# Kernel optimization log

Hardware: AMD Instinct MI355X
Metric: run time of the kernel (lower is better)

Reference implementation:

```python
import math
import jax, jax.numpy as jnp
import numpy as np

NEG = -1e32
H = 8          # n_heads
L2 = 1e-05


def _ln(x, g, b):
    m = jnp.mean(x, -1, keepdims=True)
    v = jnp.mean((x - m) ** 2, -1, keepdims=True)
    return g * (x - m) * jax.lax.rsqrt(v + 1e-5) + b


def _attn(q, k, v, gam, mask_k, zero_pad):
    # q,k,v: [B,H,S,d]; monotonic distance-decay attention (AKT style)
    d_k = q.shape[-1]
    S = q.shape[2]
    scores = jnp.einsum('bhqd,bhkd->bhqk', q, k) / math.sqrt(d_k)
    # torch: triu(ones, k=mask)==0  ->  tril(0) if mask_k==1 else tril(-1)
    mask = jnp.tril(jnp.ones((S, S), bool), 0 if mask_k == 1 else -1)[None, None]
    # first (detached) softmax, used only to build the distance effect
    s_ = jax.nn.softmax(jnp.where(mask, scores, NEG), -1) * mask
    distcum = jnp.cumsum(s_, -1)
    disttot = jnp.sum(s_, -1, keepdims=True)
    idx = jnp.arange(S, dtype=jnp.float32)
    pos = jnp.abs(idx[None, :] - idx[:, None])[None, None]  # |j - i|
    dist = jax.lax.stop_gradient(
        jnp.sqrt(jnp.clip((disttot - distcum) * pos, 0.0, None)))
    gamma = -jax.nn.softplus(gam)[None]  # [1,H,1,1], gam is learned
    total_effect = jnp.clip(jnp.exp(dist * gamma), 1e-5, 1e5)
    scores = jax.nn.softmax(jnp.where(mask, scores * total_effect, NEG), -1)
    if zero_pad:
        scores = scores.at[:, :, 0, :].set(0.0)
    return jnp.einsum('bhqk,bhkd->bhqd', scores, v)


def _mha(qi, ki, vi, kW, kb, vW, vb, oW, ob, gam, mask_k, zero_pad):
    # kq_same=True: q and k both use k_linear
    B, S = qi.shape[:2]
    sp = lambda x: x.reshape(B, S, H, -1).transpose(0, 2, 1, 3)
    q = sp(qi @ kW + kb)
    k = sp(ki @ kW + kb)
    v = sp(vi @ vW + vb)
    o = _attn(q, k, v, gam, mask_k, zero_pad)
    o = o.transpose(0, 2, 1, 3).reshape(B, S, -1)
    return o @ oW + ob


def _tlayer(query, key, values, mask_k, zero_pad, apply_pos,
            kW, kb, vW, vb, oW, ob, gam, ln1g, ln1b,
            f1W, f1b, f2W, f2b, ln2g, ln2b):
    q2 = _mha(query, key, values, kW, kb, vW, vb, oW, ob, gam, mask_k, zero_pad)
    x = _ln(query + q2, ln1g, ln1b)
    if apply_pos:
        ff = jax.nn.relu(x @ f1W + f1b) @ f2W + f2b
        x = _ln(x + ff, ln2g, ln2b)
    return x


def _forward(p_data, pa_data, target, pemb_W, diff_W, qemb_W, qemb_b,
             y_kW, y_kb, y_vW, y_vb, y_oW, y_ob, y_gam, y_ln1g, y_ln1b,
             y_f1W, y_f1b, y_f2W, y_f2b, y_ln2g, y_ln2b,
             x_kW, x_kb, x_vW, x_vb, x_oW, x_ob, x_gam, x_ln1g, x_ln1b,
             h_kW, h_kb, h_vW, h_vb, h_oW, h_ob, h_gam, h_ln1g, h_ln1b,
             h_f1W, h_f1b, h_f2W, h_f2b, h_ln2g, h_ln2b,
             oln1g, oln1b, o1W, o1b, oln2g, oln2b, o2W, o2b,
             oln3g, oln3b, o3W, o3b):
    NPID = pemb_W.shape[0] - 1

    def qe(qd):  # q_embed: Linear -> ReLU, normalized by row-sum of q_data
        return jax.nn.relu(qd @ qemb_W + qemb_b) / jnp.sum(qd, -1, keepdims=True)

    q_data = jax.nn.sigmoid(pemb_W[p_data])           # [B,S,NQ+1]
    q_embed = qe(q_data)                              # [B,S,D]
    pa_pos = jnp.where(pa_data > NPID, pa_data - NPID, 0)
    pa_neg = jnp.where(pa_data <= NPID, pa_data, 0)
    qa_pos = jax.nn.sigmoid(pemb_W[pa_pos])
    qa_neg = jax.nn.sigmoid(pemb_W[pa_neg])
    qa_embed = jnp.concatenate([qe(qa_pos), qe(qa_neg)], -1)  # [B,S,2D]
    pid = diff_W[p_data]                              # [B,S,1]
    q_embed = q_embed + pid
    qa_embed = qa_embed + pid
    c_reg = jnp.sum(pid ** 2) * L2

    # Architecture (n_blocks = 1)
    y = _tlayer(qa_embed, qa_embed, qa_embed, 1, False, True,
                y_kW, y_kb, y_vW, y_vb, y_oW, y_ob, y_gam, y_ln1g, y_ln1b,
                y_f1W, y_f1b, y_f2W, y_f2b, y_ln2g, y_ln2b)
    x = _tlayer(q_embed, q_embed, q_embed, 1, False, False,
                x_kW, x_kb, x_vW, x_vb, x_oW, x_ob, x_gam, x_ln1g, x_ln1b,
                None, None, None, None, None, None)
    x = _tlayer(x, x, y, 0, True, True,
                h_kW, h_kb, h_vW, h_vb, h_oW, h_ob, h_gam, h_ln1g, h_ln1b,
                h_f1W, h_f1b, h_f2W, h_f2b, h_ln2g, h_ln2b)

    c = jnp.concatenate([x, q_embed], -1)             # [B,S,2D]
    o = jax.nn.relu(_ln(c, oln1g, oln1b) @ o1W + o1b)
    o = jax.nn.relu(_ln(o, oln2g, oln2b) @ o2W + o2b)
    out = _ln(o, oln3g, oln3b) @ o3W + o3b            # [B,S,1]
    return out, c_reg


def setup_inputs():
    B, S, D, NQ, NPID, FC, DFF = 8, 1024, 256, 1024, 4096, 512, 2048
    key = jax.random.key(0)
    cnt = [0]

    def nk():
        cnt[0] += 1
        return jax.random.fold_in(key, cnt[0])

    def nrm(shape, s=0.05):
        return jax.random.normal(nk(), shape, dtype=jnp.float32) * s

    z = lambda sh: jnp.zeros(sh, jnp.float32)
    on = lambda sh: jnp.ones(sh, jnp.float32)

    return dict(
        p_data=jax.random.randint(nk(), (B, S), 0, NPID + 1),
        pa_data=jax.random.randint(nk(), (B, S), 0, 2 * NPID + 1),
        target=jax.random.uniform(nk(), (B, S), jnp.float32),
        pemb_W=nrm((NPID + 1, NQ + 1), 1.0), diff_W=nrm((NPID + 1, 1), 0.1),
        qemb_W=nrm((NQ + 1, D)), qemb_b=z((D,)),
        y_kW=nrm((2 * D, 2 * D)), y_kb=z((2 * D,)),
        y_vW=nrm((2 * D, 2 * D)), y_vb=z((2 * D,)),
        y_oW=nrm((2 * D, 2 * D)), y_ob=z((2 * D,)), y_gam=nrm((H, 1, 1), 1.0),
        y_ln1g=on((2 * D,)), y_ln1b=z((2 * D,)),
        y_f1W=nrm((2 * D, DFF)), y_f1b=z((DFF,)),
        y_f2W=nrm((DFF, 2 * D)), y_f2b=z((2 * D,)),
        y_ln2g=on((2 * D,)), y_ln2b=z((2 * D,)),
        x_kW=nrm((D, D)), x_kb=z((D,)), x_vW=nrm((D, D)), x_vb=z((D,)),
        x_oW=nrm((D, D)), x_ob=z((D,)), x_gam=nrm((H, 1, 1), 1.0),
        x_ln1g=on((D,)), x_ln1b=z((D,)),
        h_kW=nrm((D, D)), h_kb=z((D,)),
        h_vW=nrm((2 * D, 2 * D)), h_vb=z((2 * D,)),
        h_oW=nrm((2 * D, D)), h_ob=z((D,)), h_gam=nrm((H, 1, 1), 1.0),
        h_ln1g=on((D,)), h_ln1b=z((D,)),
        h_f1W=nrm((D, DFF)), h_f1b=z((DFF,)),
        h_f2W=nrm((DFF, D)), h_f2b=z((D,)),
        h_ln2g=on((D,)), h_ln2b=z((D,)),
        oln1g=on((2 * D,)), oln1b=z((2 * D,)),
        o1W=nrm((2 * D, FC)), o1b=z((FC,)),
        oln2g=on((FC,)), oln2b=z((FC,)),
        o2W=nrm((FC, 256)), o2b=z((256,)),
        oln3g=on((256,)), oln3b=z((256,)),
        o3W=nrm((256, 1)), o3b=z((1,)),
    )


def reference(p_data, pa_data, target, pemb_W, diff_W, qemb_W, qemb_b,
              y_kW, y_kb, y_vW, y_vb, y_oW, y_ob, y_gam, y_ln1g, y_ln1b,
              y_f1W, y_f1b, y_f2W, y_f2b, y_ln2g, y_ln2b,
              x_kW, x_kb, x_vW, x_vb, x_oW, x_ob, x_gam, x_ln1g, x_ln1b,
              h_kW, h_kb, h_vW, h_vb, h_oW, h_ob, h_gam, h_ln1g, h_ln1b,
              h_f1W, h_f1b, h_f2W, h_f2b, h_ln2g, h_ln2b,
              oln1g, oln1b, o1W, o1b, oln2g, oln2b, o2W, o2b,
              oln3g, oln3b, o3W, o3b):
    return _forward(p_data, pa_data, target, pemb_W, diff_W, qemb_W, qemb_b,
                    y_kW, y_kb, y_vW, y_vb, y_oW, y_ob, y_gam, y_ln1g, y_ln1b,
                    y_f1W, y_f1b, y_f2W, y_f2b, y_ln2g, y_ln2b,
                    x_kW, x_kb, x_vW, x_vb, x_oW, x_ob, x_gam, x_ln1g, x_ln1b,
                    h_kW, h_kb, h_vW, h_vb, h_oW, h_ob, h_gam, h_ln1g, h_ln1b,
                    h_f1W, h_f1b, h_f2W, h_f2b, h_ln2g, h_ln2b,
                    oln1g, oln1b, o1W, o1b, oln2g, oln2b, o2W, o2b,
                    oln3g, oln3b, o3W, o3b)
```

## Files before the change

### kernel.cpp

```cpp
#include <hip/hip_runtime.h>
#include <hip/hip_bf16.h>
#include <math.h>

#define NHEADS 8
#define L2E 1.44269504f

typedef __attribute__((ext_vector_type(8))) __bf16 bfrag;
typedef __attribute__((ext_vector_type(4))) float f32x4;
typedef __attribute__((ext_vector_type(8))) unsigned short u16x8;

static __device__ __forceinline__ unsigned short f2bf(float f) {
  unsigned u = __float_as_uint(f);
  unsigned r = (u + 0x7fffu + ((u >> 16) & 1u)) >> 16;
  return (unsigned short)r;
}

static __device__ __forceinline__ void gload_lds16(const void* g, void* l) {
  __builtin_amdgcn_global_load_lds(
      (const __attribute__((address_space(1))) unsigned int*)g,
      (__attribute__((address_space(3))) unsigned int*)l, 16, 0, 0);
}

static __device__ __forceinline__ float block_reduce_sum(float v, float* red) {
  int t = threadIdx.x;
  red[t] = v; __syncthreads();
  for (int s = 128; s > 0; s >>= 1) {
    if (t < s) red[t] += red[t + s];
    __syncthreads();
  }
  float r = red[0];
  __syncthreads();
  return r;
}

__global__ __launch_bounds__(256) void sig_kernel(
    const float* __restrict__ Wp, unsigned short* __restrict__ Sgb,
    float* __restrict__ Ssum, int Kd, int Kp)
{
  __shared__ float red[256];
  int row = blockIdx.x;
  float s = 0.f;
  for (int k = threadIdx.x; k < Kp; k += 256) {
    float v = 0.f;
    if (k < Kd) {
      v = 1.f / (1.f + __expf(-Wp[(size_t)row * Kd + k]));
      s += v;
    }
    Sgb[(size_t)row * Kp + k] = f2bf(v);
  }
  float tot = block_reduce_sum(s, red);
  if (threadIdx.x == 0) Ssum[row] = tot;
}

struct TDesc { const float* src; unsigned short* dst; int K, N, Kp, tilesX, blk0; };
struct TPack { TDesc d[16]; };

__global__ __launch_bounds__(256) void tconv_all_kernel(TPack P) {
  __shared__ float t[32][33];
  int bid = blockIdx.x;
  int di = 0;
  #pragma unroll
  for (int k = 1; k < 16; ++k) if (bid >= P.d[k].blk0) di = k;
  const float* src = P.d[di].src;
  unsigned short* dst = P.d[di].dst;
  int K = P.d[di].K, N = P.d[di].N, Kp = P.d[di].Kp, tilesX = P.d[di].tilesX;
  int local = bid - P.d[di].blk0;
  int bn = (local % tilesX) * 32;
  int bk = (local / tilesX) * 32;
  int tid = threadIdx.x;
  int tx = tid & 31, ty = tid >> 5;
  #pragma unroll
  for (int u = 0; u < 4; ++u) {
    int k = bk + ty + u * 8, n = bn + tx;
    t[ty + u * 8][tx] = (k < K && n < N) ? src[(size_t)k * N + n] : 0.f;
  }
  __syncthreads();
  #pragma unroll
  for (int u = 0; u < 4; ++u) {
    int n = bn + ty + u * 8, kk = bk + tx;
    if (n < N && kk < Kp)
      dst[(size_t)n * Kp + kk] = f2bf(t[tx][ty + u * 8]);
  }
}

template<int BM, int EPI, bool WF32, bool WBF, bool WTR>
__global__ __launch_bounds__(256) void mgemm_kernel(
    const unsigned short* __restrict__ A, const unsigned short* __restrict__ Bt,
    const float* __restrict__ bias, float* __restrict__ C,
    unsigned short* __restrict__ Cb, unsigned short* __restrict__ Ct,
    int M, int N, int K, const float* __restrict__ divv,
    const float* __restrict__ bias2, int Nk)
{
  constexpr int TN  = (BM == 128) ? 128 : 64;
  constexpr int NI  = (BM == 128) ? 4 : 2;
  constexpr int NJ  = (BM == 128) ? 4 : 2;
  constexpr int WSM = (BM == 128) ? 64 : 32;
  constexpr bool SPLIT = WBF && WTR;
  __shared__ __align__(16) unsigned short Als[BM * 32];
  __shared__ __align__(16) unsigned short Bls[TN * 32];
  const int tid = threadIdx.x;
  const int lane = tid & 63, w = tid >> 6;
  const int wm = w >> 1, wn = w & 1;
  const int brow = blockIdx.y * BM, bcol = blockIdx.x * TN;

  f32x4 acc[NI][NJ] = {};

  for (int k0 = 0; k0 < K; k0 += 32) {
    if constexpr (BM == 128) {
      #pragma unroll
      for (int q = 0; q < 2; ++q) {
        int s = w * 128 + q * 64 + lane;
        int r = s >> 2, g = s & 3;
        int gs = g ^ (r & 3);
        int gc = bcol + r; if (gc > N - 1) gc = N - 1;
        gload_lds16(Bt + (size_t)gc * K + k0 + gs * 8,
                    (char*)Bls + (w * 2048 + q * 1024));
      }
      #pragma unroll
      for (int q = 0; q < 2; ++q) {
        int s = w * 128 + q * 64 + lane;
        int r = s >> 2, g = s & 3;
        int gs = g ^ (r & 3);
        int gr = brow + r; if (gr > M - 1) gr = M - 1;
        gload_lds16(A + (size_t)gr * K + k0 + gs * 8,
                    (char*)Als + (w * 2048 + q * 1024));
      }
    } else {
      {
        int s = tid;
        int r = s >> 2, g = s & 3;
        int gs = g ^ (r & 3);
        int gc = bcol + r; if (gc > N - 1) gc = N - 1;
        gload_lds16(Bt + (size_t)gc * K + k0 + gs * 8,
                    (char*)Bls + w * 1024);
      }
      {
        int s = tid;
        int r = s >> 2, g = s & 3;
        int gs = g ^ (r & 3);
        int gr = brow + r; if (gr > M - 1) gr = M - 1;
        gload_lds16(A + (size_t)gr * K + k0 + gs * 8,
                    (char*)Als + w * 1024);
      }
    }
    __syncthreads();

    bfrag av[NI], bv[NJ];
    #pragma unroll
    for (int f = 0; f < NI; ++f) {
      int rA = wm * WSM + f * 16 + (lane & 15);
      av[f] = *(const bfrag*)((const char*)Als + rA * 64 + ((((lane >> 4) ^ (rA & 3))) << 4));
    }
    #pragma unroll
    for (int f = 0; f < NJ; ++f) {
      int rB = wn * WSM + f * 16 + (lane & 15);
      bv[f] = *(const bfrag*)((const char*)Bls + rB * 64 + ((((lane >> 4) ^ (rB & 3))) << 4));
    }
    #pragma unroll
    for (int i = 0; i < NI; ++i)
      #pragma unroll
      for (int j = 0; j < NJ; ++j)
        acc[i][j] = __builtin_amdgcn_mfma_f32_16x16x32_bf16(av[i], bv[j], acc[i][j], 0, 0, 0);
    __syncthreads();
  }

  #pragma unroll
  for (int i = 0; i < NI; ++i) {
    int gr0 = brow + wm * WSM + i * 16 + (lane >> 4) * 4;
    #pragma unroll
    for (int j = 0; j < NJ; ++j) {
      int gc = bcol + wn * WSM + j * 16 + (lane & 15);
      float bsv;
      if (SPLIT) bsv = (gc < Nk) ? bias[gc] : bias2[gc - Nk];
      else       bsv = bias ? bias[gc] : 0.f;
      float vv[4];
      #pragma unroll
      for (int q = 0; q < 4; ++q) {
        int gr = gr0 + q;
        float v = acc[i][j][q] + bsv;
        if (EPI >= 1) v = fmaxf(v, 0.f);
        if (EPI == 2) v = (gr < M) ? v / divv[gr] : v;
        vv[q] = v;
      }
      if (SPLIT) {
        if (gc < Nk) {
          #pragma unroll
          for (int q = 0; q < 4; ++q) {
            int gr = gr0 + q;
            if (gr < M) Cb[(size_t)gr * Nk + gc] = f2bf(vv[q]);
          }
        } else {
          ushort4 h4 = { f2bf(vv[0]), f2bf(vv[1]), f2bf(vv[2]), f2bf(vv[3]) };
          *(ushort4*)(Ct + (size_t)(gc - Nk) * M + gr0) = h4;
        }
      } else {
        #pragma unroll
        for (int q = 0; q < 4; ++q) {
          int gr = gr0 + q;
          if (gr >= M) continue;
          if (WF32) C[(size_t)gr * N + gc] = vv[q];
          if (WBF)  Cb[(size_t)gr * N + gc] = f2bf(vv[q]);
        }
        if (WTR) {
          ushort4 h4 = { f2bf(vv[0]), f2bf(vv[1]), f2bf(vv[2]), f2bf(vv[3]) };
          *(ushort4*)(Ct + (size_t)gc * M + gr0) = h4;
        }
      }
    }
  }
}

__global__ __launch_bounds__(256) void gather_kernel(
    const int* __restrict__ p_data, const int* __restrict__ pa_data,
    const float* __restrict__ E, const float* __restrict__ diff_W,
    float* __restrict__ qemb, unsigned short* __restrict__ qembb,
    float* __restrict__ qaemb, unsigned short* __restrict__ qaembb)
{
  int idx = blockIdx.x * 256 + threadIdx.x;
  if (idx >= 8192 * 512) return;
  int row = idx >> 9, c = idx & 511;
  int p = p_data[row];
  float pid = diff_W[p];
  if (c < 256) {
    float v = E[(size_t)p * 256 + c] + pid;
    qemb[(size_t)row * 256 + c] = v;
    qembb[(size_t)row * 256 + c] = f2bf(v);
  }
  int pa = pa_data[row];
  int ppos = (pa > 4096) ? pa - 4096 : 0;
  int pneg = (pa <= 4096) ? pa : 0;
  float v = (c < 256) ? E[(size_t)ppos * 256 + c] : E[(size_t)pneg * 256 + (c - 256)];
  v += pid;
  qaemb[(size_t)row * 512 + c] = v;
  qaembb[(size_t)row * 512 + c] = f2bf(v);
}

__global__ __launch_bounds__(256) void creg_kernel(
    const int* __restrict__ p_data, const float* __restrict__ dW,
    float* __restrict__ out)
{
  __shared__ float red[256];
  float s = 0.f;
  for (int i = threadIdx.x; i < 8192; i += 256) {
    float v = dW[p_data[i]];
    s += v * v;
  }
  float tot = block_reduce_sum(s, red);
  if (threadIdx.x == 0) out[0] = tot * 1e-5f;
}

template<int DK, int DV, int MASKK, int ZP>
__global__ __launch_bounds__(512, 4) void attnA_kernel(
    const unsigned short* __restrict__ QKb, const unsigned short* __restrict__ Vt,
    const float* __restrict__ gamp, unsigned short* __restrict__ O,
    int S, int MT)
{
  constexpr int RS = 1156;
  constexpr int HIOFF = 2048;
  constexpr int NPAR = (DV == 64) ? 2 : 4;
  constexpr int NFIN = (DV == 64) ? 4 : 2;
  constexpr int NP   = (DV == 32) ? 6 : 4;
  const int DMK = NHEADS * DK, DMV = NHEADS * DV;
  const int id = blockIdx.x + blockIdx.y * 64;
  const int W = (id & 7) * 512 + (id >> 3);
  const int ib = 63 - (W & 63);
  const int bh = W >> 6;
  const int i0 = ib * 16;
  const int b = bh >> 3, h = bh & 7;
  const int tid = threadIdx.x;
  const int lane = tid & 63, w = tid >> 6;
  const size_t rowbase = (size_t)b * S;

  __shared__ __align__(16) float sc[16 * RS];
  __shared__ float wrow[16];

  const int jmaxBlk = MASKK ? (i0 + 15) : (i0 + 14);
  const int NK = (jmaxBlk / 64 + 1) * 64;
  const int NKp = (NK + 255) & ~255;
  const int CD = NKp >> 5;

  const int qr = lane & 15;
  const int ko8 = (lane >> 4) * 8;
  const float rscale = rsqrtf((float)DK) * L2E;

  bfrag qf[DK / 32];
  #pragma unroll
  for (int ks = 0; ks < DK / 32; ++ks)
    qf[ks] = *(const bfrag*)(QKb + (rowbase + i0 + qr) * DMK + h * DK + ks * 32 + ko8);

  for (int t0 = 0; t0 < NK; t0 += 128) {
    int tt = t0 + (w >> 2) * 64;
    if (tt < NK) {
      int jb = tt + (w & 3) * 16 + qr;
      bfrag kf[DK / 32];
      #pragma unroll
      for (int ks = 0; ks < DK / 32; ++ks)
        kf[ks] = *(const bfrag*)(QKb + (rowbase + jb) * DMK + h * DK + ks * 32 + ko8);
      f32x4 accs = {};
      __builtin_amdgcn_s_setprio(1);
      #pragma unroll
      for (int ks = 0; ks < DK / 32; ++ks)
        accs = __builtin_amdgcn_mfma_f32_16x16x32_bf16(qf[ks], kf[ks], accs, 0, 0, 0);
      __builtin_amdgcn_s_setprio(0);
      int ja = jb + 4 * (jb >> 5);
      int r0 = (lane >> 4) * 4;
      #pragma unroll
      for (int q = 0; q < 4; ++q)
        sc[(r0 + q) * RS + ja] = accs[q] * rscale;
    }
  }
  __syncthreads();

  {
    const int g = tid >> 5, l = tid & 31;
    const int i = i0 + g;
    const int jmax = MASKK ? i : i - 1;
    const int jb0 = CD * l;

    float p[32];
    float m1 = -1e30f;
    #pragma unroll
    for (int c = 0; c < 8; ++c) {
      if (4 * c < CD) {
        int j = jb0 + 4 * c;
        f32x4 v = *(const f32x4*)(sc + g * RS + j + 4 * (j >> 5));
        #pragma unroll
        for (int k = 0; k < 4; ++k) {
          int jj = j + k;
          float s = (jj <= jmax) ? v[k] : -1e30f;
          p[4 * c + k] = s;
          m1 = fmaxf(m1, s);
        }
      }
    }
    #pragma unroll
    for (int o = 16; o > 0; o >>= 1) m1 = fmaxf(m1, __shfl_xor(m1, o, 32));

    float lloc = 0.f;
    #pragma unroll
    for (int t = 0; t < 32; ++t)
      if (t < CD) lloc += __builtin_amdgcn_exp2f(p[t] - m1);
    float l1 = lloc;
    #pragma unroll
    for (int o = 16; o > 0; o >>= 1) l1 += __shfl_xor(l1, o, 32);

    float scn = lloc;
    #pragma unroll
    for (int o = 1; o < 32; o <<= 1) {
      float u = __shfl_up(scn, o, 32);
      if (l >= o) scn += u;
    }
    float cum = scn - lloc;

    float gv = gamp[h];
    float sp = fmaxf(gv, 0.f) + log1pf(__expf(-fabsf(gv)));
    float gmr = -sp * L2E * rsqrtf(l1);
    float dj = (float)(i - jb0);
    float m2 = -1e30f;
    #pragma unroll
    for (int t = 0; t < 32; ++t) {
      if (t < CD) {
        cum += __builtin_amdgcn_exp2f(p[t] - m1);
        float rem = fmaxf(l1 - cum, 0.f);
        float dsq = sqrtf(rem * fabsf(dj));
        dj -= 1.f;
        float eff = fmaxf(__builtin_amdgcn_exp2f(gmr * dsq), 1e-5f);
        p[t] = p[t] * eff;
        m2 = fmaxf(m2, p[t]);
      }
    }
    #pragma unroll
    for (int o = 16; o > 0; o >>= 1) m2 = fmaxf(m2, __shfl_xor(m2, o, 32));

    float l2 = 0.f;
    #pragma unroll
    for (int t = 0; t < 32; ++t)
      if (t < CD) { p[t] = __builtin_amdgcn_exp2f(p[t] - m2); l2 += p[t]; }
    #pragma unroll
    for (int o = 16; o > 0; o >>= 1) l2 += __shfl_xor(l2, o, 32);
    bool validrow = (jmax >= 0) && !(ZP && i == 0);
    float wgt = validrow ? (1.f / l2) : 0.f;
    if (l == 0) wrow[g] = wgt;

    char* rowB = (char*)sc + (size_t)g * (RS * 4);
    #pragma unroll
    for (int k = 0; k < 4; ++k) {
      if (8 * k < CD) {
        int bb = (CD >> 3) * l + k;
        int pb = ((bb & 3) << 5) | (bb >> 2);
        u16x8 hi8, lo8;
        #pragma unroll
        for (int e = 0; e < 8; ++e) {
          float v = p[8 * k + e];
          __bf16 hb = (__bf16)v;
          hi8[e] = __builtin_bit_cast(unsigned short, hb);
          lo8[e] = __builtin_bit_cast(unsigned short, (__bf16)(v - (float)hb));
        }
        *(u16x8*)(rowB + 16 * pb) = hi8;
        *(u16x8*)(rowB + HIOFF + 16 * pb) = lo8;
      }
    }
  }
  __syncthreads();

  const int dblk = (DV == 64) ? (w & 3) : (w & 1);
  const int par  = (DV == 64) ? (w >> 2) : (w >> 1);
  const int dcol = h * DV + dblk * 16 + (lane & 15);
  const unsigned short* vrow = Vt + (size_t)dcol * MT + rowbase;
  f32x4 acco = {};
  const char* rowB = (const char*)sc + (size_t)qr * (RS * 4);
  __builtin_amdgcn_s_setprio(1);
  for (int t0 = par * 64; t0 < NK; t0 += NPAR * 64) {
    #pragma unroll
    for (int ks = 0; ks < 2; ++ks) {
      int jo = t0 + ks * 32 + ko8;
      int bb = jo >> 3;
      int pb = ((bb & 3) << 5) | (bb >> 2);
      bfrag ph = *(const bfrag*)(rowB + 16 * pb);
      bfrag pl = *(const bfrag*)(rowB + HIOFF + 16 * pb);
      bfrag vf = *(const bfrag*)(vrow + jo);
      acco = __builtin_amdgcn_mfma_f32_16x16x32_bf16(pl, vf, acco, 0, 0, 0);
      acco = __builtin_amdgcn_mfma_f32_16x16x32_bf16(ph, vf, acco, 0, 0, 0);
    }
  }
  __builtin_amdgcn_s_setprio(0);
  __syncthreads();

  float* redA = sc;
  if (w >= NFIN) {
    int slot = w - NFIN;
    #pragma unroll
    for (int q = 0; q < 4; ++q)
      redA[slot * 272 + ((lane >> 4) * 4 + q) * 17 + (lane & 15)] = acco[q];
  }
  __syncthreads();
  if (w < NFIN) {
    for (int pp = w; pp < NP; pp += NFIN) {
      #pragma unroll
      for (int q = 0; q < 4; ++q)
        acco[q] += redA[pp * 272 + ((lane >> 4) * 4 + q) * 17 + (lane & 15)];
    }
    int r0 = (lane >> 4) * 4;
    #pragma unroll
    for (int q = 0; q < 4; ++q) {
      float wv = wrow[r0 + q];
      O[(rowbase + i0 + r0 + q) * DMV + dcol] = f2bf(acco[q] * wv);
    }
  }
}

template<int D, bool WF, bool WB>
__global__ __launch_bounds__(256) void ln4_kernel(
    const float* __restrict__ X, const float* __restrict__ R,
    const float* __restrict__ g, const float* __restrict__ be,
    float* __restrict__ Y, unsigned short* __restrict__ Yb)
{
  constexpr int NC = D / 256;
  int row = blockIdx.x * 4 + (threadIdx.x >> 6);
  int lane = threadIdx.x & 63;
  const float* x = X + (size_t)row * D;
  f32x4 xv[NC];
  float s = 0.f;
  #pragma unroll
  for (int c = 0; c < NC; ++c) {
    xv[c] = *(const f32x4*)(x + c * 256 + lane * 4);
    if (R) {
      f32x4 rv = *(const f32x4*)(R + (size_t)row * D + c * 256 + lane * 4);
      #pragma unroll
      for (int k = 0; k < 4; ++k) xv[c][k] += rv[k];
    }
    #pragma unroll
    for (int k = 0; k < 4; ++k) s += xv[c][k];
  }
  #pragma unroll
  for (int o = 32; o > 0; o >>= 1) s += __shfl_xor(s, o, 64);
  float mean = s / (float)D;
  float vs = 0.f;
  #pragma unroll
  for (int c = 0; c < NC; ++c)
    #pragma unroll
    for (int k = 0; k < 4; ++k) { float d = xv[c][k] - mean; vs += d * d; }
  #pragma unroll
  for (int o = 32; o > 0; o >>= 1) vs += __shfl_xor(vs, o, 64);
  float rstd = rsqrtf(vs / (float)D + 1e-5f);
  #pragma unroll
  for (int c = 0; c < NC; ++c) {
    f32x4 gv = *(const f32x4*)(g + c * 256 + lane * 4);
    f32x4 bv = *(const f32x4*)(be + c * 256 + lane * 4);
    f32x4 ov;
    #pragma unroll
    for (int k = 0; k < 4; ++k) ov[k] = gv[k] * (xv[c][k] - mean) * rstd + bv[k];
    if (WF) *(f32x4*)(Y + (size_t)row * D + c * 256 + lane * 4) = ov;
    if (WB) {
      ushort4 h4 = { f2bf(ov[0]), f2bf(ov[1]), f2bf(ov[2]), f2bf(ov[3]) };
      *(ushort4*)(Yb + (size_t)row * D + c * 256 + lane * 4) = h4;
    }
  }
}

__global__ __launch_bounds__(256) void lnc_kernel(
    const float* __restrict__ Xh, const float* __restrict__ Qe,
    const float* __restrict__ g, const float* __restrict__ be,
    unsigned short* __restrict__ Yb)
{
  int row = blockIdx.x * 4 + (threadIdx.x >> 6);
  int lane = threadIdx.x & 63;
  f32x4 xv[2];
  xv[0] = *(const f32x4*)(Xh + (size_t)row * 256 + lane * 4);
  xv[1] = *(const f32x4*)(Qe + (size_t)row * 256 + lane * 4);
  float s = 0.f;
  #pragma unroll
  for (int c = 0; c < 2; ++c)
    #pragma unroll
    for (int k = 0; k < 4; ++k) s += xv[c][k];
  #pragma unroll
  for (int o = 32; o > 0; o >>= 1) s += __shfl_xor(s, o, 64);
  float mean = s / 512.f;
  float vs = 0.f;
  #pragma unroll
  for (int c = 0; c < 2; ++c)
    #pragma unroll
    for (int k = 0; k < 4; ++k) { float d = xv[c][k] - mean; vs += d * d; }
  #pragma unroll
  for (int o = 32; o > 0; o >>= 1) vs += __shfl_xor(vs, o, 64);
  float rstd = rsqrtf(vs / 512.f + 1e-5f);
  #pragma unroll
  for (int c = 0; c < 2; ++c) {
    f32x4 gv = *(const f32x4*)(g + c * 256 + lane * 4);
    f32x4 bv = *(const f32x4*)(be + c * 256 + lane * 4);
    ushort4 h4;
    #pragma unroll
    for (int k = 0; k < 4; ++k) {
      float ov = gv[k] * (xv[c][k] - mean) * rstd + bv[k];
      ((unsigned short*)&h4)[k] = f2bf(ov);
    }
    *(ushort4*)(Yb + (size_t)row * 512 + c * 256 + lane * 4) = h4;
  }
}

__global__ __launch_bounds__(256) void lndot_kernel(
    const float* __restrict__ X, const float* __restrict__ g,
    const float* __restrict__ be, const float* __restrict__ w3,
    const float* __restrict__ b3, float* __restrict__ out)
{
  int row = blockIdx.x * 4 + (threadIdx.x >> 6);
  int lane = threadIdx.x & 63;
  f32x4 v = *(const f32x4*)(X + (size_t)row * 256 + lane * 4);
  float s = v[0] + v[1] + v[2] + v[3];
  #pragma unroll
  for (int o = 32; o > 0; o >>= 1) s += __shfl_xor(s, o, 64);
  float mean = s / 256.f;
  float vs = 0.f;
  #pragma unroll
  for (int k = 0; k < 4; ++k) { float d = v[k] - mean; vs += d * d; }
  #pragma unroll
  for (int o = 32; o > 0; o >>= 1) vs += __shfl_xor(vs, o, 64);
  float rstd = rsqrtf(vs / 256.f + 1e-5f);
  f32x4 gv = *(const f32x4*)(g + lane * 4);
  f32x4 bv = *(const f32x4*)(be + lane * 4);
  f32x4 wv = *(const f32x4*)(w3 + lane * 4);
  float d = 0.f;
  #pragma unroll
  for (int k = 0; k < 4; ++k)
    d += (gv[k] * (v[k] - mean) * rstd + bv[k]) * wv[k];
  #pragma unroll
  for (int o = 32; o > 0; o >>= 1) d += __shfl_xor(d, o, 64);
  if (lane == 0) out[row] = d + b3[0];
}

extern "C" void kernel_launch(void* const* d_in, const int* in_sizes, int n_in,
                              void* d_out, int out_size, void* d_ws, size_t ws_size,
                              hipStream_t stream) {
  const int* p_data  = (const int*)d_in[0];
  const int* pa_data = (const int*)d_in[1];
  const float* pemb_W = (const float*)d_in[3];
  const float* diff_W = (const float*)d_in[4];
  const float* qemb_W = (const float*)d_in[5];
  const float* qemb_b = (const float*)d_in[6];
  const float* y_kW = (const float*)d_in[7];   const float* y_kb = (const float*)d_in[8];
  const float* y_vW = (const float*)d_in[9];   const float* y_vb = (const float*)d_in[10];
  const float* y_oW = (const float*)d_in[11];  const float* y_ob = (const float*)d_in[12];
  const float* y_gam = (const float*)d_in[13];
  const float* y_ln1g = (const float*)d_in[14]; const float* y_ln1b = (const float*)d_in[15];
  const float* y_f1W = (const float*)d_in[16]; const float* y_f1b = (const float*)d_in[17];
  const float* y_f2W = (const float*)d_in[18]; const float* y_f2b = (const float*)d_in[19];
  const float* y_ln2g = (const float*)d_in[20]; const float* y_ln2b = (const float*)d_in[21];
  const float* x_kW = (const float*)d_in[22];  const float* x_kb = (const float*)d_in[23];
  const float* x_vW = (const float*)d_in[24];  const float* x_vb = (const float*)d_in[25];
  const float* x_oW = (const float*)d_in[26];  const float* x_ob = (const float*)d_in[27];
  const float* x_gam = (const float*)d_in[28];
  const float* x_ln1g = (const float*)d_in[29]; const float* x_ln1b = (const float*)d_in[30];
  const float* h_kW = (const float*)d_in[31];  const float* h_kb = (const float*)d_in[32];
  const float* h_vW = (const float*)d_in[33];  const float* h_vb = (const float*)d_in[34];
  const float* h_oW = (const float*)d_in[35];  const float* h_ob = (const float*)d_in[36];
  const float* h_gam = (const float*)d_in[37];
  const float* h_ln1g = (const float*)d_in[38]; const float* h_ln1b = (const float*)d_in[39];
  const float* h_f1W = (const float*)d_in[40]; const float* h_f1b = (const float*)d_in[41];
  const float* h_f2W = (const float*)d_in[42]; const float* h_f2b = (const float*)d_in[43];
  const float* h_ln2g = (const float*)d_in[44]; const float* h_ln2b = (const float*)d_in[45];
  const float* oln1g = (const float*)d_in[46]; const float* oln1b = (const float*)d_in[47];
  const float* o1W = (const float*)d_in[48];   const float* o1b = (const float*)d_in[49];
  const float* oln2g = (const float*)d_in[50]; const float* oln2b = (const float*)d_in[51];
  const float* o2W = (const float*)d_in[52];   const float* o2b = (const float*)d_in[53];
  const float* oln3g = (const float*)d_in[54]; const float* oln3b = (const float*)d_in[55];
  const float* o3W = (const float*)d_in[56];   const float* o3b = (const float*)d_in[57];

  float* out_f = (float*)d_out;

  const int B = 8, S = 1024, M = B * S;
  const int R = 4097, KQ = 1025, KQP = 1056;

  float* ws = (float*)d_ws;
  size_t off = 0;
  auto alloc = [&](size_t nfloats) { size_t o = off; off += (nfloats + 255) & ~(size_t)255; return o; };
  auto allocs = [&](size_t nshorts) { return alloc((nshorts + 1) / 2); };

  size_t oE    = alloc((size_t)R * 256);
  size_t oSIGb = allocs((size_t)R * KQP);
  size_t oSSUM = alloc(R);
  size_t oQE   = alloc((size_t)M * 256);
  size_t oQEb  = allocs((size_t)M * 256);
  size_t oQA   = alloc((size_t)M * 512);
  size_t oQAb  = allocs((size_t)M * 512);
  size_t oYOb  = allocs((size_t)M * 512);
  size_t oXO   = alloc((size_t)M * 256);
  size_t oXOb  = allocs((size_t)M * 256);
  size_t oHO   = alloc((size_t)M * 256);
  size_t oS0   = alloc((size_t)M * 512);
  size_t oS1   = alloc((size_t)M * 512);
  size_t oS2b  = allocs((size_t)M * 512);
  size_t oS3   = alloc((size_t)M * 512);
  size_t oS4   = alloc((size_t)M * 512);
  size_t oSX   = alloc((size_t)M * 512);
  size_t oSXb  = allocs((size_t)M * 512);
  size_t oS0b  = allocs((size_t)M * 512);
  size_t oVt   = allocs((size_t)M * 512);
  size_t oWqe  = allocs((size_t)256 * KQP);
  size_t oWyk  = allocs((size_t)512 * 512);
  size_t oWyv  = allocs((size_t)512 * 512);
  size_t oWyo  = allocs((size_t)512 * 512);
  size_t oWyf1 = allocs((size_t)2048 * 512);
  size_t oWyf2 = allocs((size_t)512 * 2048);
  size_t oWxk  = allocs((size_t)256 * 256);
  size_t oWxv  = allocs((size_t)256 * 256);
  size_t oWxo  = allocs((size_t)256 * 256);
  size_t oWhk  = allocs((size_t)256 * 256);
  size_t oWhv  = allocs((size_t)512 * 512);
  size_t oWho  = allocs((size_t)256 * 512);
  size_t oWhf1 = allocs((size_t)2048 * 256);
  size_t oWhf2 = allocs((size_t)256 * 2048);
  size_t oWo1  = allocs((size_t)512 * 512);
  size_t oWo2  = allocs((size_t)256 * 512);
  (void)ws_size; (void)in_sizes; (void)n_in; (void)out_size;

  float* E    = ws + oE;
  unsigned short* SIGb = (unsigned short*)(ws + oSIGb);
  float* SSUM = ws + oSSUM;
  float* QE   = ws + oQE;   unsigned short* QEb = (unsigned short*)(ws + oQEb);
  float* QA   = ws + oQA;   unsigned short* QAb = (unsigned short*)(ws + oQAb);
  unsigned short* YOb = (unsigned short*)(ws + oYOb);
  float* XO   = ws + oXO;   unsigned short* XOb = (unsigned short*)(ws + oXOb);
  float* HO   = ws + oHO;
  float* S0   = ws + oS0;
  unsigned short* S2b = (unsigned short*)(ws + oS2b);
  float* S3   = ws + oS3;
  float* S4   = ws + oS4;
  float* SX   = ws + oSX;   unsigned short* SXb = (unsigned short*)(ws + oSXb);
  unsigned short* S0b = (unsigned short*)(ws + oS0b);
  unsigned short* Vt  = (unsigned short*)(ws + oVt);
  unsigned short* FFb = (unsigned short*)S0;

  unsigned short* Wqe  = (unsigned short*)(ws + oWqe);
  unsigned short* Wyk  = (unsigned short*)(ws + oWyk);
  unsigned short* Wyv  = (unsigned short*)(ws + oWyv);
  unsigned short* Wyo  = (unsigned short*)(ws + oWyo);
  unsigned short* Wyf1 = (unsigned short*)(ws + oWyf1);
  unsigned short* Wyf2 = (unsigned short*)(ws + oWyf2);
  unsigned short* Wxk  = (unsigned short*)(ws + oWxk);
  unsigned short* Wxv  = (unsigned short*)(ws + oWxv);
  unsigned short* Wxo  = (unsigned short*)(ws + oWxo);
  unsigned short* Whk  = (unsigned short*)(ws + oWhk);
  unsigned short* Whv  = (unsigned short*)(ws + oWhv);
  unsigned short* Who  = (unsigned short*)(ws + oWho);
  unsigned short* Whf1 = (unsigned short*)(ws + oWhf1);
  unsigned short* Whf2 = (unsigned short*)(ws + oWhf2);
  unsigned short* Wo1  = (unsigned short*)(ws + oWo1);
  unsigned short* Wo2  = (unsigned short*)(ws + oWo2);

  dim3 blk(256);
  int nElem512 = (8192 * 512 + 255) / 256;

  {
    struct HD { const float* src; unsigned short* dst; int K, N, Kp; };
    const HD hd[16] = {
      {qemb_W, Wqe, KQ, 256, KQP},
      {y_kW, Wyk, 512, 512, 512}, {y_vW, Wyv, 512, 512, 512}, {y_oW, Wyo, 512, 512, 512},
      {y_f1W, Wyf1, 512, 2048, 512}, {y_f2W, Wyf2, 2048, 512, 2048},
      {x_kW, Wxk, 256, 256, 256}, {x_vW, Wxv, 256, 256, 256}, {x_oW, Wxo, 256, 256, 256},
      {h_kW, Whk, 256, 256, 256}, {h_vW, Whv, 512, 512, 512}, {h_oW, Who, 512, 256, 512},
      {h_f1W, Whf1, 256, 2048, 256}, {h_f2W, Whf2, 2048, 256, 2048},
      {o1W, Wo1, 512, 512, 512}, {o2W, Wo2, 512, 256, 512},
    };
    TPack P;
    int tot = 0;
    for (int k = 0; k < 16; ++k) {
      int tx = (hd[k].N + 31) / 32, ty = (hd[k].Kp + 31) / 32;
      P.d[k] = { hd[k].src, hd[k].dst, hd[k].K, hd[k].N, hd[k].Kp, tx, tot };
      tot += tx * ty;
    }
    tconv_all_kernel<<<dim3(tot), blk, 0, stream>>>(P);
  }

  auto gg128 = [](int Mm, int Nn) { return dim3((unsigned)(Nn / 128), (unsigned)((Mm + 127) / 128)); };
  auto gg64  = [](int Mm, int Nn) { return dim3((unsigned)(Nn / 64), (unsigned)((Mm + 63) / 64)); };

  sig_kernel<<<R, blk, 0, stream>>>(pemb_W, SIGb, SSUM, KQ, KQP);
  mgemm_kernel<64, 2, true, false, false><<<gg64(R, 256), blk, 0, stream>>>(SIGb, Wqe, qemb_b, E, nullptr, nullptr, R, 256, KQP, SSUM, nullptr, 0);
  gather_kernel<<<nElem512, blk, 0, stream>>>(p_data, pa_data, E, diff_W, QE, QEb, QA, QAb);
  creg_kernel<<<1, blk, 0, stream>>>(p_data, diff_W, out_f + 8192);

  dim3 ablk(512);
  dim3 lgrid(M / 4);
  dim3 agA(64, B * NHEADS);

  mgemm_kernel<64, 0, false, true, true><<<gg64(M, 1024), blk, 0, stream>>>(QAb, Wyk, y_kb, nullptr, S0b, Vt, M, 1024, 512, nullptr, y_vb, 512);
  attnA_kernel<64, 64, 1, 0><<<agA, ablk, 0, stream>>>(S0b, Vt, y_gam, S2b, S, M);
  mgemm_kernel<64, 0, true, false, false><<<gg64(M, 512), blk, 0, stream>>>(S2b, Wyo, y_ob, S3, nullptr, nullptr, M, 512, 512, nullptr, nullptr, 0);
  ln4_kernel<512, true, true><<<lgrid, blk, 0, stream>>>(QA, S3, y_ln1g, y_ln1b, SX, SXb);
  mgemm_kernel<128, 1, false, true, false><<<gg128(M, 2048), blk, 0, stream>>>(SXb, Wyf1, y_f1b, nullptr, FFb, nullptr, M, 2048, 512, nullptr, nullptr, 0);
  mgemm_kernel<128, 0, true, false, false><<<gg128(M, 512), blk, 0, stream>>>(FFb, Wyf2, y_f2b, S4, nullptr, nullptr, M, 512, 2048, nullptr, nullptr, 0);
  ln4_kernel<512, false, true><<<lgrid, blk, 0, stream>>>(SX, S4, y_ln2g, y_ln2b, nullptr, YOb);

  mgemm_kernel<64, 0, false, true, true><<<gg64(M, 512), blk, 0, stream>>>(QEb, Wxk, x_kb, nullptr, S0b, Vt, M, 512, 256, nullptr, x_vb, 256);
  attnA_kernel<32, 32, 1, 0><<<agA, ablk, 0, stream>>>(S0b, Vt, x_gam, S2b, S, M);
  mgemm_kernel<64, 0, true, false, false><<<gg64(M, 256), blk, 0, stream>>>(S2b, Wxo, x_ob, S3, nullptr, nullptr, M, 256, 256, nullptr, nullptr, 0);
  ln4_kernel<256, true, true><<<lgrid, blk, 0, stream>>>(QE, S3, x_ln1g, x_ln1b, XO, XOb);

  mgemm_kernel<64, 0, false, true, false><<<gg64(M, 256), blk, 0, stream>>>(XOb, Whk, h_kb, nullptr, S0b, nullptr, M, 256, 256, nullptr, nullptr, 0);
  mgemm_kernel<64, 0, false, false, true><<<gg64(M, 512), blk, 0, stream>>>(YOb, Whv, h_vb, nullptr, nullptr, Vt, M, 512, 512, nullptr, nullptr, 0);
  attnA_kernel<32, 64, 0, 1><<<agA, ablk, 0, stream>>>(S0b, Vt, h_gam, S2b, S, M);
  mgemm_kernel<64, 0, true, false, false><<<gg64(M, 256), blk, 0, stream>>>(S2b, Who, h_ob, S3, nullptr, nullptr, M, 256, 512, nullptr, nullptr, 0);
  ln4_kernel<256, true, true><<<lgrid, blk, 0, stream>>>(XO, S3, h_ln1g, h_ln1b, SX, SXb);
  mgemm_kernel<128, 1, false, true, false><<<gg128(M, 2048), blk, 0, stream>>>(SXb, Whf1, h_f1b, nullptr, FFb, nullptr, M, 2048, 256, nullptr, nullptr, 0);
  mgemm_kernel<64, 0, true, false, false><<<gg64(M, 256), blk, 0, stream>>>(FFb, Whf2, h_f2b, S4, nullptr, nullptr, M, 256, 2048, nullptr, nullptr, 0);
  ln4_kernel<256, true, false><<<lgrid, blk, 0, stream>>>(SX, S4, h_ln2g, h_ln2b, HO, nullptr);

  lnc_kernel<<<lgrid, blk, 0, stream>>>(HO, QE, oln1g, oln1b, SXb);
  mgemm_kernel<64, 1, true, false, false><<<gg64(M, 512), blk, 0, stream>>>(SXb, Wo1, o1b, S3, nullptr, nullptr, M, 512, 512, nullptr, nullptr, 0);
  ln4_kernel<512, false, true><<<lgrid, blk, 0, stream>>>(S3, nullptr, oln2g, oln2b, nullptr, SXb);
  mgemm_kernel<64, 1, true, false, false><<<gg64(M, 256), blk, 0, stream>>>(SXb, Wo2, o2b, S4, nullptr, nullptr, M, 256, 512, nullptr, nullptr, 0);
  lndot_kernel<<<lgrid, blk, 0, stream>>>(S4, oln3g, oln3b, o3W, o3b, out_f);
}
```

Baseline: 747.8 us.

## Stream attention softmax through LDS and add 128x64 GEMM tile shape

The attention kernel no longer holds the per-row score array in registers. It rereads scores from shared memory in each softmax pass, writes the decayed scores back in place, and then stores the bf16 hi/lo probabilities interleaved in the same row buffer. The aim is to cut register pressure and the separate packed-layout region, at the cost of more LDS traffic. The GEMM template also gains an independent TN parameter, so several projections now use 128x64 tiles instead of 64x64, which changes per-block reuse and grid size.

```diff
diff --git a/kernel.cpp b/kernel.cpp
--- a/kernel.cpp
+++ b/kernel.cpp
@@ -83,7 +83,7 @@
   }
 }
 
-template<int BM, int EPI, bool WF32, bool WBF, bool WTR>
+template<int BM, int TN, int EPI, bool WF32, bool WBF, bool WTR>
 __global__ __launch_bounds__(256) void mgemm_kernel(
     const unsigned short* __restrict__ A, const unsigned short* __restrict__ Bt,
     const float* __restrict__ bias, float* __restrict__ C,
@@ -91,10 +91,8 @@
     int M, int N, int K, const float* __restrict__ divv,
     const float* __restrict__ bias2, int Nk)
 {
-  constexpr int TN  = (BM == 128) ? 128 : 64;
-  constexpr int NI  = (BM == 128) ? 4 : 2;
-  constexpr int NJ  = (BM == 128) ? 4 : 2;
-  constexpr int WSM = (BM == 128) ? 64 : 32;
+  constexpr int NI = BM / 32, NJ = TN / 32;
+  constexpr int WR = BM / 2, WC = TN / 2;
   constexpr bool SPLIT = WBF && WTR;
   __shared__ __align__(16) unsigned short Als[BM * 32];
   __shared__ __align__(16) unsigned short Bls[TN * 32];
@@ -106,7 +104,7 @@
   f32x4 acc[NI][NJ] = {};
 
   for (int k0 = 0; k0 < K; k0 += 32) {
-    if constexpr (BM == 128) {
+    if constexpr (TN == 128) {
       #pragma unroll
       for (int q = 0; q < 2; ++q) {
         int s = w * 128 + q * 64 + lane;
@@ -116,6 +114,15 @@
         gload_lds16(Bt + (size_t)gc * K + k0 + gs * 8,
                     (char*)Bls + (w * 2048 + q * 1024));
       }
+    } else {
+      int s = tid;
+      int r = s >> 2, g = s & 3;
+      int gs = g ^ (r & 3);
+      int gc = bcol + r; if (gc > N - 1) gc = N - 1;
+      gload_lds16(Bt + (size_t)gc * K + k0 + gs * 8,
+                  (char*)Bls + w * 1024);
+    }
+    if constexpr (BM == 128) {
       #pragma unroll
       for (int q = 0; q < 2; ++q) {
         int s = w * 128 + q * 64 + lane;
@@ -126,34 +133,24 @@
                     (char*)Als + (w * 2048 + q * 1024));
       }
     } else {
-      {
-        int s = tid;
-        int r = s >> 2, g = s & 3;
-        int gs = g ^ (r & 3);
-        int gc = bcol + r; if (gc > N - 1) gc = N - 1;
-        gload_lds16(Bt + (size_t)gc * K + k0 + gs * 8,
-                    (char*)Bls + w * 1024);
-      }
-      {
-        int s = tid;
-        int r = s >> 2, g = s & 3;
-        int gs = g ^ (r & 3);
-        int gr = brow + r; if (gr > M - 1) gr = M - 1;
-        gload_lds16(A + (size_t)gr * K + k0 + gs * 8,
-                    (char*)Als + w * 1024);
-      }
+      int s = tid;
+      int r = s >> 2, g = s & 3;
+      int gs = g ^ (r & 3);
+      int gr = brow + r; if (gr > M - 1) gr = M - 1;
+      gload_lds16(A + (size_t)gr * K + k0 + gs * 8,
+                  (char*)Als + w * 1024);
     }
     __syncthreads();
 
     bfrag av[NI], bv[NJ];
     #pragma unroll
     for (int f = 0; f < NI; ++f) {
-      int rA = wm * WSM + f * 16 + (lane & 15);
+      int rA = wm * WR + f * 16 + (lane & 15);
       av[f] = *(const bfrag*)((const char*)Als + rA * 64 + ((((lane >> 4) ^ (rA & 3))) << 4));
     }
     #pragma unroll
     for (int f = 0; f < NJ; ++f) {
-      int rB = wn * WSM + f * 16 + (lane & 15);
+      int rB = wn * WC + f * 16 + (lane & 15);
       bv[f] = *(const bfrag*)((const char*)Bls + rB * 64 + ((((lane >> 4) ^ (rB & 3))) << 4));
     }
     #pragma unroll
@@ -166,10 +163,10 @@
 
   #pragma unroll
   for (int i = 0; i < NI; ++i) {
-    int gr0 = brow + wm * WSM + i * 16 + (lane >> 4) * 4;
+    int gr0 = brow + wm * WR + i * 16 + (lane >> 4) * 4;
     #pragma unroll
     for (int j = 0; j < NJ; ++j) {
-      int gc = bcol + wn * WSM + j * 16 + (lane & 15);
+      int gc = bcol + wn * WC + j * 16 + (lane & 15);
       float bsv;
       if (SPLIT) bsv = (gc < Nk) ? bias[gc] : bias2[gc - Nk];
       else       bsv = bias ? bias[gc] : 0.f;
@@ -250,13 +247,12 @@
 }
 
 template<int DK, int DV, int MASKK, int ZP>
-__global__ __launch_bounds__(512, 4) void attnA_kernel(
+__global__ __launch_bounds__(512, 4) void attnB_kernel(
     const unsigned short* __restrict__ QKb, const unsigned short* __restrict__ Vt,
     const float* __restrict__ gamp, unsigned short* __restrict__ O,
     int S, int MT)
 {
   constexpr int RS = 1156;
-  constexpr int HIOFF = 2048;
   constexpr int NPAR = (DV == 64) ? 2 : 4;
   constexpr int NFIN = (DV == 64) ? 4 : 2;
   constexpr int NP   = (DV == 32) ? 6 : 4;
@@ -316,30 +312,28 @@
     const int i = i0 + g;
     const int jmax = MASKK ? i : i - 1;
     const int jb0 = CD * l;
-
-    float p[32];
+    const int CD4 = CD >> 2, CD8 = CD >> 3;
+    float* rowF = sc + g * RS;
+
     float m1 = -1e30f;
-    #pragma unroll
-    for (int c = 0; c < 8; ++c) {
-      if (4 * c < CD) {
-        int j = jb0 + 4 * c;
-        f32x4 v = *(const f32x4*)(sc + g * RS + j + 4 * (j >> 5));
-        #pragma unroll
-        for (int k = 0; k < 4; ++k) {
-          int jj = j + k;
-          float s = (jj <= jmax) ? v[k] : -1e30f;
-          p[4 * c + k] = s;
-          m1 = fmaxf(m1, s);
-        }
-      }
+    for (int c = 0; c < CD4; ++c) {
+      int j = jb0 + 4 * c;
+      f32x4 v = *(const f32x4*)(rowF + j + 4 * (j >> 5));
+      #pragma unroll
+      for (int k = 0; k < 4; ++k)
+        m1 = fmaxf(m1, (j + k <= jmax) ? v[k] : -1e30f);
     }
     #pragma unroll
     for (int o = 16; o > 0; o >>= 1) m1 = fmaxf(m1, __shfl_xor(m1, o, 32));
 
     float lloc = 0.f;
-    #pragma unroll
-    for (int t = 0; t < 32; ++t)
-      if (t < CD) lloc += __builtin_amdgcn_exp2f(p[t] - m1);
+    for (int c = 0; c < CD4; ++c) {
+      int j = jb0 + 4 * c;
+      f32x4 v = *(const f32x4*)(rowF + j + 4 * (j >> 5));
+      #pragma unroll
+      for (int k = 0; k < 4; ++k)
+        lloc += (j + k <= jmax) ? __builtin_amdgcn_exp2f(v[k] - m1) : 0.f;
+    }
     float l1 = lloc;
     #pragma unroll
     for (int o = 16; o > 0; o >>= 1) l1 += __shfl_xor(l1, o, 32);
@@ -355,51 +349,62 @@
     float gv = gamp[h];
     float sp = fmaxf(gv, 0.f) + log1pf(__expf(-fabsf(gv)));
     float gmr = -sp * L2E * rsqrtf(l1);
-    float dj = (float)(i - jb0);
+
     float m2 = -1e30f;
-    #pragma unroll
-    for (int t = 0; t < 32; ++t) {
-      if (t < CD) {
-        cum += __builtin_amdgcn_exp2f(p[t] - m1);
+    for (int c = 0; c < CD4; ++c) {
+      int j = jb0 + 4 * c;
+      float* ap = rowF + j + 4 * (j >> 5);
+      f32x4 v = *(const f32x4*)ap;
+      f32x4 ov;
+      #pragma unroll
+      for (int k = 0; k < 4; ++k) {
+        int jj = j + k;
+        bool ok = jj <= jmax;
+        float e1 = ok ? __builtin_amdgcn_exp2f(v[k] - m1) : 0.f;
+        cum += e1;
         float rem = fmaxf(l1 - cum, 0.f);
-        float dsq = sqrtf(rem * fabsf(dj));
-        dj -= 1.f;
+        float dsq = sqrtf(rem * fabsf((float)(i - jj)));
         float eff = fmaxf(__builtin_amdgcn_exp2f(gmr * dsq), 1e-5f);
-        p[t] = p[t] * eff;
-        m2 = fmaxf(m2, p[t]);
+        float pv = ok ? v[k] * eff : -1e30f;
+        ov[k] = pv;
+        m2 = fmaxf(m2, pv);
       }
+      *(f32x4*)ap = ov;
     }
     #pragma unroll
     for (int o = 16; o > 0; o >>= 1) m2 = fmaxf(m2, __shfl_xor(m2, o, 32));
 
     float l2 = 0.f;
-    #pragma unroll
-    for (int t = 0; t < 32; ++t)
-      if (t < CD) { p[t] = __builtin_amdgcn_exp2f(p[t] - m2); l2 += p[t]; }
+    for (int m = 0; m < CD8; ++m) {
+      int jo = jb0 + 8 * m;
+      char* base = (char*)(rowF + jo + 4 * (jo >> 5));
+      f32x4 a = *(const f32x4*)base;
+      f32x4 bq = *(const f32x4*)(base + 16);
+      u16x8 hi8, lo8;
+      #pragma unroll
+      for (int e = 0; e < 4; ++e) {
+        float ev = __builtin_amdgcn_exp2f(a[e] - m2);
+        l2 += ev;
+        __bf16 hb = (__bf16)ev;
+        hi8[e] = __builtin_bit_cast(unsigned short, hb);
+        lo8[e] = __builtin_bit_cast(unsigned short, (__bf16)(ev - (float)hb));
+      }
+      #pragma unroll
+      for (int e = 0; e < 4; ++e) {
+        float ev = __builtin_amdgcn_exp2f(bq[e] - m2);
+        l2 += ev;
+        __bf16 hb = (__bf16)ev;
+        hi8[4 + e] = __builtin_bit_cast(unsigned short, hb);
+        lo8[4 + e] = __builtin_bit_cast(unsigned short, (__bf16)(ev - (float)hb));
+      }
+      *(u16x8*)base = hi8;
+      *(u16x8*)(base + 16) = lo8;
+    }
     #pragma unroll
     for (int o = 16; o > 0; o >>= 1) l2 += __shfl_xor(l2, o, 32);
     bool validrow = (jmax >= 0) && !(ZP && i == 0);
     float wgt = validrow ? (1.f / l2) : 0.f;
     if (l == 0) wrow[g] = wgt;
-
-    char* rowB = (char*)sc + (size_t)g * (RS * 4);
-    #pragma unroll
-    for (int k = 0; k < 4; ++k) {
-      if (8 * k < CD) {
-        int bb = (CD >> 3) * l + k;
-        int pb = ((bb & 3) << 5) | (bb >> 2);
-        u16x8 hi8, lo8;
-        #pragma unroll
-        for (int e = 0; e < 8; ++e) {
-          float v = p[8 * k + e];
-          __bf16 hb = (__bf16)v;
-          hi8[e] = __builtin_bit_cast(unsigned short, hb);
-          lo8[e] = __builtin_bit_cast(unsigned short, (__bf16)(v - (float)hb));
-        }
-        *(u16x8*)(rowB + 16 * pb) = hi8;
-        *(u16x8*)(rowB + HIOFF + 16 * pb) = lo8;
-      }
-    }
   }
   __syncthreads();
 
@@ -408,16 +413,15 @@
   const int dcol = h * DV + dblk * 16 + (lane & 15);
   const unsigned short* vrow = Vt + (size_t)dcol * MT + rowbase;
   f32x4 acco = {};
-  const char* rowB = (const char*)sc + (size_t)qr * (RS * 4);
+  const float* rowF = sc + qr * RS;
   __builtin_amdgcn_s_setprio(1);
   for (int t0 = par * 64; t0 < NK; t0 += NPAR * 64) {
     #pragma unroll
     for (int ks = 0; ks < 2; ++ks) {
       int jo = t0 + ks * 32 + ko8;
-      int bb = jo >> 3;
-      int pb = ((bb & 3) << 5) | (bb >> 2);
-      bfrag ph = *(const bfrag*)(rowB + 16 * pb);
-      bfrag pl = *(const bfrag*)(rowB + HIOFF + 16 * pb);
+      const char* base = (const char*)(rowF + jo + 4 * (jo >> 5));
+      bfrag ph = *(const bfrag*)base;
+      bfrag pl = *(const bfrag*)(base + 16);
       bfrag vf = *(const bfrag*)(vrow + jo);
       acco = __builtin_amdgcn_mfma_f32_16x16x32_bf16(pl, vf, acco, 0, 0, 0);
       acco = __builtin_amdgcn_mfma_f32_16x16x32_bf16(ph, vf, acco, 0, 0, 0);
@@ -711,11 +715,12 @@
     tconv_all_kernel<<<dim3(tot), blk, 0, stream>>>(P);
   }
 
-  auto gg128 = [](int Mm, int Nn) { return dim3((unsigned)(Nn / 128), (unsigned)((Mm + 127) / 128)); };
-  auto gg64  = [](int Mm, int Nn) { return dim3((unsigned)(Nn / 64), (unsigned)((Mm + 63) / 64)); };
+  auto gg = [](int BMv, int TNv, int Mm, int Nn) {
+    return dim3((unsigned)(Nn / TNv), (unsigned)((Mm + BMv - 1) / BMv));
+  };
 
   sig_kernel<<<R, blk, 0, stream>>>(pemb_W, SIGb, SSUM, KQ, KQP);
-  mgemm_kernel<64, 2, true, false, false><<<gg64(R, 256), blk, 0, stream>>>(SIGb, Wqe, qemb_b, E, nullptr, nullptr, R, 256, KQP, SSUM, nullptr, 0);
+  mgemm_kernel<64, 64, 2, true, false, false><<<gg(64, 64, R, 256), blk, 0, stream>>>(SIGb, Wqe, qemb_b, E, nullptr, nullptr, R, 256, KQP, SSUM, nullptr, 0);
   gather_kernel<<<nElem512, blk, 0, stream>>>(p_data, pa_data, E, diff_W, QE, QEb, QA, QAb);
   creg_kernel<<<1, blk, 0, stream>>>(p_data, diff_W, out_f + 8192);
 
@@ -723,31 +728,31 @@
   dim3 lgrid(M / 4);
   dim3 agA(64, B * NHEADS);
 
-  mgemm_kernel<64, 0, false, true, true><<<gg64(M, 1024), blk, 0, stream>>>(QAb, Wyk, y_kb, nullptr, S0b, Vt, M, 1024, 512, nullptr, y_vb, 512);
-  attnA_kernel<64, 64, 1, 0><<<agA, ablk, 0, stream>>>(S0b, Vt, y_gam, S2b, S, M);
-  mgemm_kernel<64, 0, true, false, false><<<gg64(M, 512), blk, 0, stream>>>(S2b, Wyo, y_ob, S3, nullptr, nullptr, M, 512, 512, nullptr, nullptr, 0);
+  mgemm_kernel<128, 64, 0, false, true, true><<<gg(128, 64, M, 1024), blk, 0, stream>>>(QAb, Wyk, y_kb, nullptr, S0b, Vt, M, 1024, 512, nullptr, y_vb, 512);
+  attnB_kernel<64, 64, 1, 0><<<agA, ablk, 0, stream>>>(S0b, Vt, y_gam, S2b, S, M);
+  mgemm_kernel<128, 64, 0, true, false, false><<<gg(128, 64, M, 512), blk, 0, stream>>>(S2b, Wyo, y_ob, S3, nullptr, nullptr, M, 512, 512, nullptr, nullptr, 0);
   ln4_kernel<512, true, true><<<lgrid, blk, 0, stream>>>(QA, S3, y_ln1g, y_ln1b, SX, SXb);
-  mgemm_kernel<128, 1, false, true, false><<<gg128(M, 2048), blk, 0, stream>>>(SXb, Wyf1, y_f1b, nullptr, FFb, nullptr, M, 2048, 512, nullptr, nullptr, 0);
-  mgemm_kernel<128, 0, true, false, false><<<gg128(M, 512), blk, 0, stream>>>(FFb, Wyf2, y_f2b, S4, nullptr, nullptr, M, 512, 2048, nullptr, nullptr, 0);
+  mgemm_kernel<128, 128, 1, false, true, false><<<gg(128, 128, M, 2048), blk, 0, stream>>>(SXb, Wyf1, y_f1b, nullptr, FFb, nullptr, M, 2048, 512, nullptr, nullptr, 0);
+  mgemm_kernel<128, 128, 0, true, false, false><<<gg(128, 128, M, 512), blk, 0, stream>>>(FFb, Wyf2, y_f2b, S4, nullptr, nullptr, M, 512, 2048, nullptr, nullptr, 0);
   ln4_kernel<512, false, true><<<lgrid, blk, 0, stream>>>(SX, S4, y_ln2g, y_ln2b, nullptr, YOb);
 
-  mgemm_kernel<64, 0, false, true, true><<<gg64(M, 512), blk, 0, stream>>>(QEb, Wxk, x_kb, nullptr, S0b, Vt, M, 512, 256, nullptr, x_vb, 256);
-  attnA_kernel<32, 32, 1, 0><<<agA, ablk, 0, stream>>>(S0b, Vt, x_gam, S2b, S, M);
-  mgemm_kernel<64, 0, true, false, false><<<gg64(M, 256), blk, 0, stream>>>(S2b, Wxo, x_ob, S3, nullptr, nullptr, M, 256, 256, nullptr, nullptr, 0);
+  mgemm_kernel<128, 64, 0, false, true, true><<<gg(128, 64, M, 512), blk, 0, stream>>>(QEb, Wxk, x_kb, nullptr, S0b, Vt, M, 512, 256, nullptr, x_vb, 256);
+  attnB_kernel<32, 32, 1, 0><<<agA, ablk, 0, stream>>>(S0b, Vt, x_gam, S2b, S, M);
+  mgemm_kernel<64, 64, 0, true, false, false><<<gg(64, 64, M, 256), blk, 0, stream>>>(S2b, Wxo, x_ob, S3, nullptr, nullptr, M, 256, 256, nullptr, nullptr, 0);
   ln4_kernel<256, true, true><<<lgrid, blk, 0, stream>>>(QE, S3, x_ln1g, x_ln1b, XO, XOb);
 
-  mgemm_kernel<64, 0, false, true, false><<<gg64(M, 256), blk, 0, stream>>>(XOb, Whk, h_kb, nullptr, S0b, nullptr, M, 256, 256, nullptr, nullptr, 0);
-  mgemm_kernel<64, 0, false, false, true><<<gg64(M, 512), blk, 0, stream>>>(YOb, Whv, h_vb, nullptr, nullptr, Vt, M, 512, 512, nullptr, nullptr, 0);
-  attnA_kernel<32, 64, 0, 1><<<agA, ablk, 0, stream>>>(S0b, Vt, h_gam, S2b, S, M);
-  mgemm_kernel<64, 0, true, false, false><<<gg64(M, 256), blk, 0, stream>>>(S2b, Who, h_ob, S3, nullptr, nullptr, M, 256, 512, nullptr, nullptr, 0);
+  mgemm_kernel<64, 64, 0, false, true, false><<<gg(64, 64, M, 256), blk, 0, stream>>>(XOb, Whk, h_kb, nullptr, S0b, nullptr, M, 256, 256, nullptr, nullptr, 0);
+  mgemm_kernel<128, 64, 0, false, false, true><<<gg(128, 64, M, 512), blk, 0, stream>>>(YOb, Whv, h_vb, nullptr, nullptr, Vt, M, 512, 512, nullptr, nullptr, 0);
+  attnB_kernel<32, 64, 0, 1><<<agA, ablk, 0, stream>>>(S0b, Vt, h_gam, S2b, S, M);
+  mgemm_kernel<64, 64, 0, true, false, false><<<gg(64, 64, M, 256), blk, 0, stream>>>(S2b, Who, h_ob, S3, nullptr, nullptr, M, 256, 512, nullptr, nullptr, 0);
   ln4_kernel<256, true, true><<<lgrid, blk, 0, stream>>>(XO, S3, h_ln1g, h_ln1b, SX, SXb);
-  mgemm_kernel<128, 1, false, true, false><<<gg128(M, 2048), blk, 0, stream>>>(SXb, Whf1, h_f1b, nullptr, FFb, nullptr, M, 2048, 256, nullptr, nullptr, 0);
-  mgemm_kernel<64, 0, true, false, false><<<gg64(M, 256), blk, 0, stream>>>(FFb, Whf2, h_f2b, S4, nullptr, nullptr, M, 256, 2048, nullptr, nullptr, 0);
+  mgemm_kernel<128, 128, 1, false, true, false><<<gg(128, 128, M, 2048), blk, 0, stream>>>(SXb, Whf1, h_f1b, nullptr, FFb, nullptr, M, 2048, 256, nullptr, nullptr, 0);
+  mgemm_kernel<64, 64, 0, true, false, false><<<gg(64, 64, M, 256), blk, 0, stream>>>(FFb, Whf2, h_f2b, S4, nullptr, nullptr, M, 256, 2048, nullptr, nullptr, 0);
   ln4_kernel<256, true, false><<<lgrid, blk, 0, stream>>>(SX, S4, h_ln2g, h_ln2b, HO, nullptr);
 
   lnc_kernel<<<lgrid, blk, 0, stream>>>(HO, QE, oln1g, oln1b, SXb);
-  mgemm_kernel<64, 1, true, false, false><<<gg64(M, 512), blk, 0, stream>>>(SXb, Wo1, o1b, S3, nullptr, nullptr, M, 512, 512, nullptr, nullptr, 0);
+  mgemm_kernel<128, 64, 1, true, false, false><<<gg(128, 64, M, 512), blk, 0, stream>>>(SXb, Wo1, o1b, S3, nullptr, nullptr, M, 512, 512, nullptr, nullptr, 0);
   ln4_kernel<512, false, true><<<lgrid, blk, 0, stream>>>(S3, nullptr, oln2g, oln2b, nullptr, SXb);
-  mgemm_kernel<64, 1, true, false, false><<<gg64(M, 256), blk, 0, stream>>>(SXb, Wo2, o2b, S4, nullptr, nullptr, M, 256, 512, nullptr, nullptr, 0);
+  mgemm_kernel<64, 64, 1, true, false, false><<<gg(64, 64, M, 256), blk, 0, stream>>>(SXb, Wo2, o2b, S4, nullptr, nullptr, M, 256, 512, nullptr, nullptr, 0);
   lndot_kernel<<<lgrid, blk, 0, stream>>>(S4, oln3g, oln3b, o3W, o3b, out_f);
 }
```

Measured after the change: 747.7 us. Within noise of the previous version (-0.0%).
